# Performance work log

Hardware: AMD Instinct MI355X
Metric: run time of the kernel (lower is better)

Reference implementation:

```python
import jax, jax.numpy as jnp
import numpy as np

B, N, P, D = 16, 1024, 72, 96
ND, H, K = 64, 4, 16
LN_EPS = 1e-5
ROW_EPS = 1e-8


def topk_sparsify(adj, k):
    # adj: (..., N, N); keep top-k per row (scatter-mask), then row-renormalize
    shp = adj.shape
    n = shp[-1]
    flat = adj.reshape(-1, n)
    _, idx = jax.lax.top_k(flat, k)  # (R, k)
    rows = jnp.arange(flat.shape[0])[:, None]
    mask = jnp.zeros_like(flat).at[rows, idx].set(1.0)
    sp = flat * mask
    sp = sp / (sp.sum(-1, keepdims=True) + ROW_EPS)
    return sp.reshape(shp)


def setup_inputs() -> dict:
    key = jax.random.key(0)
    ks = jax.random.split(key, 12)
    xav1 = np.sqrt(6.0 / (N + ND))  # xavier_uniform bound for (N, ND)
    inp = {
        "patch_features": jax.random.normal(ks[0], (B, N, P, D), jnp.float32),
        "E1": jax.random.uniform(ks[1], (H, N, ND), jnp.float32, -xav1, xav1),
        "E2": jax.random.uniform(ks[2], (H, ND, N), jnp.float32, -xav1, xav1),
        "temperature": jnp.full((H,), 0.5, jnp.float32),
        "fusion_weight": jnp.float32(0.5),
        "dW1": jax.random.normal(ks[3], (D, ND), jnp.float32) / np.sqrt(D),
        "db1": jnp.zeros((ND,), jnp.float32),
        "ln_g": jnp.ones((ND,), jnp.float32),
        "ln_b": jnp.zeros((ND,), jnp.float32),
        "dW2": jax.random.normal(ks[4], (ND, ND), jnp.float32) / np.sqrt(ND),
        "db2": jnp.zeros((ND,), jnp.float32),
        "eW1": jax.random.normal(ks[5], (H, 2 * H), jnp.float32) / np.sqrt(H),
        "eb1": jnp.zeros((2 * H,), jnp.float32),
        "eW2": jax.random.normal(ks[6], (2 * H, 1), jnp.float32) / np.sqrt(2 * H),
        "eb2": jnp.zeros((1,), jnp.float32),
    }
    return inp


def reference(patch_features, E1, E2, temperature, fusion_weight,
              dW1, db1, ln_g, ln_b, dW2, db2, eW1, eb1, eW2, eb2):
    # ---- static multi-head graphs: softmax(relu(E1 @ E2) / T, axis=-1) ----
    s = jax.nn.relu(jnp.einsum('hnd,hdm->hnm', E1, E2))
    static_adjs = jax.nn.softmax(s / temperature[:, None, None], axis=-1)

    # ---- dynamic graphs from mean-pooled patch features ----
    node_repr = patch_features.mean(axis=2)                 # (B, N, D)
    h1 = node_repr @ dW1 + db1                              # (B, N, ND)
    mu = h1.mean(-1, keepdims=True)
    var = ((h1 - mu) ** 2).mean(-1, keepdims=True)
    h1 = (h1 - mu) / jnp.sqrt(var + LN_EPS) * ln_g + ln_b   # LayerNorm
    h1 = jax.nn.relu(h1)                                    # (dropout = identity, eval)
    dyn_emb = h1 @ dW2 + db2                                # (B, N, ND)
    d = jax.nn.relu(jnp.einsum('bnd,hdm->bhnm', dyn_emb, E2))
    dynamic_adjs = jax.nn.softmax(d / temperature[None, :, None, None], axis=-1)

    # ---- top-k sparsify + row renormalize ----
    static_adjs = topk_sparsify(static_adjs, K)             # (H, N, N)
    dynamic_adjs = topk_sparsify(dynamic_adjs, K)           # (B, H, N, N)

    # ---- fuse static + dynamic ----
    fused = (1.0 - fusion_weight) * static_adjs[None] + fusion_weight * dynamic_adjs

    # ---- edge MLP over head dim: (B, N, N, H) -> (B, N, N) ----
    x = jnp.transpose(fused, (0, 2, 3, 1))                  # (B, N, N, H)
    ew = jax.nn.relu(x @ eW1 + eb1) @ eW2 + eb2             # (B, N, N, 1)
    final_adjs = jax.nn.sigmoid(ew[..., 0]) * fused.mean(axis=1)
    return final_adjs, static_adjs, dynamic_adjs
```

## Files before the change

### kernel.cpp

```cpp
#include <hip/hip_runtime.h>

typedef unsigned int u32;
typedef unsigned long long u64;
typedef unsigned short u16;

#define Bn 16
#define Nn 1024
#define Pp 72
#define MARG 3e-4f

#define NEGINF __int_as_float(0xff800000)
#define POSINF __int_as_float(0x7f800000)

__device__ __forceinline__ float wsumf(float v) {
#pragma unroll
  for (int off = 1; off < 64; off <<= 1) v += __shfl_xor(v, off, 64);
  return v;
}
__device__ __forceinline__ float wmaxf(float v) {
#pragma unroll
  for (int off = 1; off < 64; off <<= 1) v = fmaxf(v, __shfl_xor(v, off, 64));
  return v;
}
__device__ __forceinline__ float wminf(float v) {
#pragma unroll
  for (int off = 1; off < 64; off <<= 1) v = fminf(v, __shfl_xor(v, off, 64));
  return v;
}
__device__ __forceinline__ u32 wminu(u32 v) {
#pragma unroll
  for (int off = 1; off < 64; off <<= 1) {
    u32 o = (u32)__shfl_xor((int)v, off, 64);
    v = (o < v) ? o : v;
  }
  return v;
}

__global__ __launch_bounds__(256) void k_e2t(const float* __restrict__ E2,
                                             float* __restrict__ E2T) {
  __shared__ float tile[32][65];
  const int h = blockIdx.x >> 5;
  const int m0 = (blockIdx.x & 31) << 5;
  const float* src = E2 + (size_t)h * 65536;
  float* dst = E2T + (size_t)h * 65536;
  const int t = threadIdx.x;
#pragma unroll
  for (int k = 0; k < 8; ++k) {
    int idx = k * 256 + t;
    int d = idx >> 5, mm = idx & 31;
    tile[mm][d] = src[d * 1024 + m0 + mm];
  }
  __syncthreads();
#pragma unroll
  for (int k = 0; k < 8; ++k) {
    int idx = k * 256 + t;
    int mm = idx >> 6, d = idx & 63;
    dst[(size_t)(m0 + mm) * 64 + d] = tile[mm][d];
  }
}

__global__ __launch_bounds__(128) void k_meanmlp(const float* __restrict__ pf,
                                                 const float* __restrict__ dW1,
                                                 const float* __restrict__ db1,
                                                 const float* __restrict__ ln_g,
                                                 const float* __restrict__ ln_b,
                                                 const float* __restrict__ dW2,
                                                 const float* __restrict__ db2,
                                                 double* __restrict__ embD,
                                                 float* __restrict__ embF) {
  __shared__ double ndD[96];
  __shared__ double red[64];
  __shared__ double h1r[64];
  const int t = threadIdx.x;
  const int bn = blockIdx.x;

  if (t < 96) {
    const float* src = pf + (size_t)bn * (Pp * 96) + t;
    double s = 0.0;
    for (int p = 0; p < Pp; ++p) s += (double)src[p * 96];
    ndD[t] = s / 72.0;
  }
  __syncthreads();

  double a = 0.0;
  if (t < 64) {
    a = (double)db1[t];
    for (int d = 0; d < 96; ++d) a = fma(ndD[d], (double)dW1[d * 64 + t], a);
    red[t] = a;
  }
  __syncthreads();
  for (int s2 = 32; s2 >= 1; s2 >>= 1) {
    if (t < s2) red[t] += red[t + s2];
    __syncthreads();
  }
  const double mu = red[0] * (1.0 / 64.0);
  __syncthreads();
  const double dv = a - mu;
  if (t < 64) red[t] = dv * dv;
  __syncthreads();
  for (int s2 = 32; s2 >= 1; s2 >>= 1) {
    if (t < s2) red[t] += red[t + s2];
    __syncthreads();
  }
  const double var = red[0] * (1.0 / 64.0);
  if (t < 64) {
    double xn = dv / sqrt(var + 1e-5) * (double)ln_g[t] + (double)ln_b[t];
    h1r[t] = xn > 0.0 ? xn : 0.0;
  }
  __syncthreads();
  if (t < 64) {
    double e = (double)db2[t];
    for (int k = 0; k < 64; ++k) e = fma(h1r[k], (double)dW2[k * 64 + t], e);
    embD[(size_t)bn * 64 + t] = e;
    embF[(size_t)bn * 64 + t] = (float)e;
  }
}

template <int MODE>
__global__ __launch_bounds__(256) void k_rows(const float* __restrict__ e1f,
                                              const double* __restrict__ embD,
                                              const float* __restrict__ embF,
                                              const float* __restrict__ E2,
                                              const float* __restrict__ E2T,
                                              const float* __restrict__ temp,
                                              float* __restrict__ outp) {
  __shared__ float lgA[8][1024];
  __shared__ float embsh[64][8];
  const int t = threadIdx.x;
  const int r0 = blockIdx.x * 8;
  int h;
  size_t erow;
  if (MODE == 0) {
    h = r0 >> 10;
    erow = (size_t)r0;
  } else {
    int b = r0 >> 12;
    h = (r0 >> 10) & 3;
    int n0 = r0 & 1023;
    erow = (size_t)(b << 10) + n0;
  }
  const float* efa = (MODE == 0) ? (e1f + erow * 64) : (embF + erow * 64);
  const float4* e2 = (const float4*)(E2 + (size_t)h * 65536);
  const float* e2t = E2T + (size_t)h * 65536;
  const float invT = 1.0f / temp[h];
  const double Td = (double)temp[h];

  for (int k = t; k < 512; k += 256) {
    int g = k & 7, d = k >> 3;
    embsh[d][g] = efa[g * 64 + d];
  }
  __syncthreads();

  float acc[8][4];
#pragma unroll
  for (int g = 0; g < 8; ++g)
#pragma unroll
    for (int x = 0; x < 4; ++x) acc[g][x] = 0.0f;

#pragma unroll 2
  for (int d = 0; d < 64; ++d) {
    float4 ev = e2[d * 256 + t];
    float4 sa = *(const float4*)&embsh[d][0];
    float4 sb = *(const float4*)&embsh[d][4];
    acc[0][0] = fmaf(sa.x, ev.x, acc[0][0]);
    acc[0][1] = fmaf(sa.x, ev.y, acc[0][1]);
    acc[0][2] = fmaf(sa.x, ev.z, acc[0][2]);
    acc[0][3] = fmaf(sa.x, ev.w, acc[0][3]);
    acc[1][0] = fmaf(sa.y, ev.x, acc[1][0]);
    acc[1][1] = fmaf(sa.y, ev.y, acc[1][1]);
    acc[1][2] = fmaf(sa.y, ev.z, acc[1][2]);
    acc[1][3] = fmaf(sa.y, ev.w, acc[1][3]);
    acc[2][0] = fmaf(sa.z, ev.x, acc[2][0]);
    acc[2][1] = fmaf(sa.z, ev.y, acc[2][1]);
    acc[2][2] = fmaf(sa.z, ev.z, acc[2][2]);
    acc[2][3] = fmaf(sa.z, ev.w, acc[2][3]);
    acc[3][0] = fmaf(sa.w, ev.x, acc[3][0]);
    acc[3][1] = fmaf(sa.w, ev.y, acc[3][1]);
    acc[3][2] = fmaf(sa.w, ev.z, acc[3][2]);
    acc[3][3] = fmaf(sa.w, ev.w, acc[3][3]);
    acc[4][0] = fmaf(sb.x, ev.x, acc[4][0]);
    acc[4][1] = fmaf(sb.x, ev.y, acc[4][1]);
    acc[4][2] = fmaf(sb.x, ev.z, acc[4][2]);
    acc[4][3] = fmaf(sb.x, ev.w, acc[4][3]);
    acc[5][0] = fmaf(sb.y, ev.x, acc[5][0]);
    acc[5][1] = fmaf(sb.y, ev.y, acc[5][1]);
    acc[5][2] = fmaf(sb.y, ev.z, acc[5][2]);
    acc[5][3] = fmaf(sb.y, ev.w, acc[5][3]);
    acc[6][0] = fmaf(sb.z, ev.x, acc[6][0]);
    acc[6][1] = fmaf(sb.z, ev.y, acc[6][1]);
    acc[6][2] = fmaf(sb.z, ev.z, acc[6][2]);
    acc[6][3] = fmaf(sb.z, ev.w, acc[6][3]);
    acc[7][0] = fmaf(sb.w, ev.x, acc[7][0]);
    acc[7][1] = fmaf(sb.w, ev.y, acc[7][1]);
    acc[7][2] = fmaf(sb.w, ev.z, acc[7][2]);
    acc[7][3] = fmaf(sb.w, ev.w, acc[7][3]);
  }
#pragma unroll
  for (int g = 0; g < 8; ++g) {
    float4 o;
    o.x = fmaxf(acc[g][0], 0.0f) * invT;
    o.y = fmaxf(acc[g][1], 0.0f) * invT;
    o.z = fmaxf(acc[g][2], 0.0f) * invT;
    o.w = fmaxf(acc[g][3], 0.0f) * invT;
    ((float4*)(&lgA[g][0]))[t] = o;
  }
  __syncthreads();

  const int w = t >> 6, l = t & 63;

#pragma unroll 1
  for (int gi = 0; gi < 2; ++gi) {
    const int g = w * 2 + gi;
    float q[16];
#pragma unroll
    for (int j = 0; j < 16; ++j) q[j] = lgA[g][l + (j << 6)];

    float lm = q[0];
#pragma unroll
    for (int j = 1; j < 16; ++j) lm = fmaxf(lm, q[j]);
    const float qmax = wmaxf(lm);

    u32 lo = 0u, hi = __float_as_uint(qmax) + 1u;
    u32 kept = 0u;
    bool f16 = false;
    float pvf = 0.0f;
#pragma unroll 1
    while (hi - lo > 1u) {
      u32 mid = (lo + hi) >> 1;
      float pv = __uint_as_float(mid);
      u32 cw = 0;
#pragma unroll
      for (int j = 0; j < 16; ++j)
        cw += (u32)__popcll(__ballot(q[j] >= pv));
      if (cw >= 16u) lo = mid; else hi = mid;
      if (cw == 16u) { f16 = true; pvf = pv; break; }
    }
    float theta, ub;
    if (f16) {
      float vmin = POSINF, umax = -1.0f;
#pragma unroll
      for (int j = 0; j < 16; ++j) {
        if (q[j] >= pvf) { kept |= 1u << j; vmin = fminf(vmin, q[j]); }
        else umax = fmaxf(umax, q[j]);
      }
      theta = wminf(vmin);
      ub = wmaxf(umax);
    } else {
      theta = __uint_as_float(lo);
      u32 cw = 0;
#pragma unroll
      for (int j = 0; j < 16; ++j) {
        u64 bj = __ballot(q[j] > theta);
        cw += (u32)__popcll(bj);
        if (q[j] > theta) kept |= 1u << j;
      }
      int r = 16 - (int)cw;
#pragma unroll 1
      for (int it = 0; it < r; ++it) {
        u32 mc = 0xFFFFFFFFu;
#pragma unroll
        for (int j = 0; j < 16; ++j)
          if (q[j] == theta && !((kept >> j) & 1u)) {
            u32 cc = (u32)((j << 6) | l);
            mc = cc < mc ? cc : mc;
          }
        u32 wm = wminu(mc);
        if ((wm & 63u) == (u32)l) kept |= 1u << (wm >> 6);
      }
      ub = theta;
    }

    if (theta - ub >= MARG) {
      float e[16];
      float es = 0.0f, ek = 0.0f;
#pragma unroll
      for (int j = 0; j < 16; ++j) {
        e[j] = __expf(q[j] - qmax);
        es += e[j];
        if ((kept >> j) & 1u) ek += e[j];
      }
      const float Z = wsumf(es);
      const float EK = wsumf(ek);
      const float inv = 1.0f / (EK + 1e-8f * Z);
#pragma unroll
      for (int j = 0; j < 16; ++j)
        lgA[g][l + (j << 6)] = ((kept >> j) & 1u) ? (e[j] * inv) : 0.0f;
    } else {
      double qd[16];
      const float thr = ub - MARG;
#pragma unroll 1
      for (int j = 0; j < 16; ++j) {
        if (q[j] >= thr) {
          const int m = l + (j << 6);
          const float* col = e2t + (size_t)m * 64;
          double a = 0.0;
          for (int d = 0; d < 64; ++d) {
            double s = (MODE == 0) ? (double)e1f[(erow + g) * 64 + d]
                                   : embD[(erow + g) * 64 + d];
            a = fma(s, (double)col[d], a);
          }
          qd[j] = (a > 0.0 ? a : 0.0) / Td;
        } else {
          qd[j] = (double)q[j];
        }
      }
      double bm = qd[0];
#pragma unroll
      for (int j = 1; j < 16; ++j) bm = qd[j] > bm ? qd[j] : bm;
      float mh = (float)bm;
      float mlo = (float)(bm - (double)mh);
      float whi = wmaxf(mh);
      float wlo = wmaxf(mh == whi ? mlo : NEGINF);
      const double qmaxd = (double)whi + (double)wlo;

      float ev2[16];
      float es2 = 0.0f;
#pragma unroll
      for (int j = 0; j < 16; ++j) { ev2[j] = __expf((float)(qd[j] - qmaxd)); es2 += ev2[j]; }
      const float Z2 = wsumf(es2);

      u32 kept2 = 0;
      float EK2 = 0.0f;
#pragma unroll 1
      for (int it = 0; it < 16; ++it) {
        double bv = -1.0;
        int bjj = -1;
#pragma unroll
        for (int j = 0; j < 16; ++j) {
          bool tk = (((kept2 >> j) & 1u) == 0u) && (qd[j] > bv);
          bv = tk ? qd[j] : bv;
          bjj = tk ? j : bjj;
        }
        float bh = NEGINF, bl = NEGINF;
        if (bjj >= 0) { bh = (float)bv; bl = (float)(bv - (double)bh); }
        float vhi = wmaxf(bh);
        float vlo = wmaxf(bh == vhi ? bl : NEGINF);
        bool elig = (bh == vhi) && (bl == vlo);
        u32 mc = elig ? (u32)((bjj << 6) | l) : 0xFFFFFFFFu;
        u32 mwin = wminu(mc);
        EK2 += __expf((float)(((double)vhi + (double)vlo) - qmaxd));
        if ((mwin & 63u) == (u32)l) kept2 |= 1u << (mwin >> 6);
      }
      const float inv2 = 1.0f / (EK2 + 1e-8f * Z2);
#pragma unroll
      for (int j = 0; j < 16; ++j)
        lgA[g][l + (j << 6)] = ((kept2 >> j) & 1u) ? (ev2[j] * inv2) : 0.0f;
    }
  }
  __syncthreads();

  float4* gout = (float4*)(outp + (size_t)r0 * 1024);
  const float4* src = (const float4*)(&lgA[0][0]);
#pragma unroll
  for (int k = 0; k < 8; ++k) {
    int i = t + k * 256;
    gout[i] = src[i];
  }
}

__global__ __launch_bounds__(256) void k_fuse(const float* __restrict__ dyn,
                                              const float* __restrict__ stat,
                                              float* __restrict__ fin,
                                              const float* __restrict__ eW1,
                                              const float* __restrict__ eb1,
                                              const float* __restrict__ eW2,
                                              const float* __restrict__ eb2,
                                              const float* __restrict__ fwp) {
  const float w = fwp[0];
  const float w1 = 1.0f - w;
  float W1[4][8], B1v[8], W2v[8];
#pragma unroll
  for (int hh = 0; hh < 4; ++hh)
#pragma unroll
    for (int j = 0; j < 8; ++j) W1[hh][j] = eW1[hh * 8 + j];
#pragma unroll
  for (int j = 0; j < 8; ++j) { B1v[j] = eb1[j]; W2v[j] = eW2[j]; }
  const float b2 = eb2[0];

  const int i = blockIdx.x * 256 + threadIdx.x;
  const int b = i >> 18;
  const int rem = i & 262143;
  const int n = rem >> 8;
  const int c4 = rem & 255;

  float fx[4][4];
#pragma unroll
  for (int hh = 0; hh < 4; ++hh) {
    float4 fd = ((const float4*)dyn)[(((size_t)((b * 4 + hh) * 1024 + n)) << 8) + c4];
    float4 fs = ((const float4*)stat)[(((size_t)(hh * 1024 + n)) << 8) + c4];
    fx[hh][0] = w1 * fs.x + w * fd.x;
    fx[hh][1] = w1 * fs.y + w * fd.y;
    fx[hh][2] = w1 * fs.z + w * fd.z;
    fx[hh][3] = w1 * fs.w + w * fd.w;
  }
  float ov[4];
#pragma unroll
  for (int x = 0; x < 4; ++x) {
    float ew = b2;
#pragma unroll
    for (int j = 0; j < 8; ++j) {
      float hj = B1v[j];
#pragma unroll
      for (int hh = 0; hh < 4; ++hh) hj = fmaf(fx[hh][x], W1[hh][j], hj);
      ew = fmaf(fmaxf(hj, 0.0f), W2v[j], ew);
    }
    float mean = (fx[0][x] + fx[1][x] + fx[2][x] + fx[3][x]) * 0.25f;
    float sg = 1.0f / (1.0f + __expf(-ew));
    ov[x] = sg * mean;
  }
  float4 o;
  o.x = ov[0]; o.y = ov[1]; o.z = ov[2]; o.w = ov[3];
  ((float4*)fin)[i] = o;
}

extern "C" void kernel_launch(void* const* d_in, const int* in_sizes, int n_in,
                              void* d_out, int out_size, void* d_ws, size_t ws_size,
                              hipStream_t stream) {
  const float* pf   = (const float*)d_in[0];
  const float* E1   = (const float*)d_in[1];
  const float* E2   = (const float*)d_in[2];
  const float* temp = (const float*)d_in[3];
  const float* fw   = (const float*)d_in[4];
  const float* dW1  = (const float*)d_in[5];
  const float* db1  = (const float*)d_in[6];
  const float* ln_g = (const float*)d_in[7];
  const float* ln_b = (const float*)d_in[8];
  const float* dW2  = (const float*)d_in[9];
  const float* db2  = (const float*)d_in[10];
  const float* eW1  = (const float*)d_in[11];
  const float* eb1  = (const float*)d_in[12];
  const float* eW2  = (const float*)d_in[13];
  const float* eb2  = (const float*)d_in[14];

  float* out_final = (float*)d_out;
  float* out_stat  = out_final + (size_t)Bn * Nn * Nn;
  float* out_dyn   = out_stat + (size_t)4 * Nn * Nn;

  double* embD = (double*)d_out;
  float* embF = out_final + 2097152;
  float* E2T  = out_final + 3145728;

  k_e2t<<<128, 256, 0, stream>>>(E2, E2T);
  k_meanmlp<<<Bn * Nn, 128, 0, stream>>>(pf, dW1, db1, ln_g, ln_b, dW2, db2, embD, embF);
  k_rows<0><<<512, 256, 0, stream>>>(E1, nullptr, nullptr, E2, E2T, temp, out_stat);
  k_rows<1><<<8192, 256, 0, stream>>>(nullptr, embD, embF, E2, E2T, temp, out_dyn);
  k_fuse<<<16384, 256, 0, stream>>>(out_dyn, out_stat, out_final, eW1, eb1, eW2, eb2, fw);
}
```

Before: 662.8 us.

## Use 512-thread row blocks with one row per wave and DPP reductions

```diff
diff --git a/kernel.cpp b/kernel.cpp
--- a/kernel.cpp
+++ b/kernel.cpp
@@ -12,21 +12,28 @@
 #define NEGINF __int_as_float(0xff800000)
 #define POSINF __int_as_float(0x7f800000)
 
-__device__ __forceinline__ float wsumf(float v) {
-#pragma unroll
-  for (int off = 1; off < 64; off <<= 1) v += __shfl_xor(v, off, 64);
-  return v;
-}
-__device__ __forceinline__ float wmaxf(float v) {
-#pragma unroll
-  for (int off = 1; off < 64; off <<= 1) v = fmaxf(v, __shfl_xor(v, off, 64));
-  return v;
-}
-__device__ __forceinline__ float wminf(float v) {
-#pragma unroll
-  for (int off = 1; off < 64; off <<= 1) v = fminf(v, __shfl_xor(v, off, 64));
-  return v;
-}
+#define DPP_STEP(OP, CTRL, RM)                                                 \
+  y = __builtin_amdgcn_update_dpp(__float_as_int(v), __float_as_int(v),        \
+                                  CTRL, RM, 0xf, false);                       \
+  v = OP(v, __int_as_float(y));
+
+#define DPP_RED(NAME, OP)                                                      \
+  __device__ __forceinline__ float NAME(float v) {                             \
+    int y;                                                                     \
+    DPP_STEP(OP, 0x111, 0xf)                                                   \
+    DPP_STEP(OP, 0x112, 0xf)                                                   \
+    DPP_STEP(OP, 0x114, 0xf)                                                   \
+    DPP_STEP(OP, 0x118, 0xf)                                                   \
+    DPP_STEP(OP, 0x142, 0xa)                                                   \
+    DPP_STEP(OP, 0x143, 0xc)                                                   \
+    return __int_as_float(__builtin_amdgcn_readlane(__float_as_int(v), 63));   \
+  }
+
+#define FADDOP(a, b) ((a) + (b))
+DPP_RED(dmaxf, fmaxf)
+DPP_RED(dminf, fminf)
+DPP_RED(dsumf, FADDOP)
+
 __device__ __forceinline__ u32 wminu(u32 v) {
 #pragma unroll
   for (int off = 1; off < 64; off <<= 1) {
@@ -117,7 +124,7 @@
 }
 
 template <int MODE>
-__global__ __launch_bounds__(256) void k_rows(const float* __restrict__ e1f,
+__global__ __launch_bounds__(512) void k_rows(const float* __restrict__ e1f,
                                               const double* __restrict__ embD,
                                               const float* __restrict__ embF,
                                               const float* __restrict__ E2,
@@ -140,77 +147,55 @@
     erow = (size_t)(b << 10) + n0;
   }
   const float* efa = (MODE == 0) ? (e1f + erow * 64) : (embF + erow * 64);
-  const float4* e2 = (const float4*)(E2 + (size_t)h * 65536);
+  const float2* e2 = (const float2*)(E2 + (size_t)h * 65536);
   const float* e2t = E2T + (size_t)h * 65536;
   const float invT = 1.0f / temp[h];
   const double Td = (double)temp[h];
 
-  for (int k = t; k < 512; k += 256) {
-    int g = k & 7, d = k >> 3;
+  {
+    int g = t & 7, d = t >> 3;
     embsh[d][g] = efa[g * 64 + d];
   }
   __syncthreads();
 
-  float acc[8][4];
-#pragma unroll
-  for (int g = 0; g < 8; ++g)
-#pragma unroll
-    for (int x = 0; x < 4; ++x) acc[g][x] = 0.0f;
-
-#pragma unroll 2
+  float acc[8][2];
+#pragma unroll
+  for (int g = 0; g < 8; ++g) { acc[g][0] = 0.0f; acc[g][1] = 0.0f; }
+
+#pragma unroll 4
   for (int d = 0; d < 64; ++d) {
-    float4 ev = e2[d * 256 + t];
+    float2 ev = e2[d * 512 + t];
     float4 sa = *(const float4*)&embsh[d][0];
     float4 sb = *(const float4*)&embsh[d][4];
     acc[0][0] = fmaf(sa.x, ev.x, acc[0][0]);
     acc[0][1] = fmaf(sa.x, ev.y, acc[0][1]);
-    acc[0][2] = fmaf(sa.x, ev.z, acc[0][2]);
-    acc[0][3] = fmaf(sa.x, ev.w, acc[0][3]);
     acc[1][0] = fmaf(sa.y, ev.x, acc[1][0]);
     acc[1][1] = fmaf(sa.y, ev.y, acc[1][1]);
-    acc[1][2] = fmaf(sa.y, ev.z, acc[1][2]);
-    acc[1][3] = fmaf(sa.y, ev.w, acc[1][3]);
     acc[2][0] = fmaf(sa.z, ev.x, acc[2][0]);
     acc[2][1] = fmaf(sa.z, ev.y, acc[2][1]);
-    acc[2][2] = fmaf(sa.z, ev.z, acc[2][2]);
-    acc[2][3] = fmaf(sa.z, ev.w, acc[2][3]);
     acc[3][0] = fmaf(sa.w, ev.x, acc[3][0]);
     acc[3][1] = fmaf(sa.w, ev.y, acc[3][1]);
-    acc[3][2] = fmaf(sa.w, ev.z, acc[3][2]);
-    acc[3][3] = fmaf(sa.w, ev.w, acc[3][3]);
     acc[4][0] = fmaf(sb.x, ev.x, acc[4][0]);
     acc[4][1] = fmaf(sb.x, ev.y, acc[4][1]);
-    acc[4][2] = fmaf(sb.x, ev.z, acc[4][2]);
-    acc[4][3] = fmaf(sb.x, ev.w, acc[4][3]);
     acc[5][0] = fmaf(sb.y, ev.x, acc[5][0]);
     acc[5][1] = fmaf(sb.y, ev.y, acc[5][1]);
-    acc[5][2] = fmaf(sb.y, ev.z, acc[5][2]);
-    acc[5][3] = fmaf(sb.y, ev.w, acc[5][3]);
     acc[6][0] = fmaf(sb.z, ev.x, acc[6][0]);
     acc[6][1] = fmaf(sb.z, ev.y, acc[6][1]);
-    acc[6][2] = fmaf(sb.z, ev.z, acc[6][2]);
-    acc[6][3] = fmaf(sb.z, ev.w, acc[6][3]);
     acc[7][0] = fmaf(sb.w, ev.x, acc[7][0]);
     acc[7][1] = fmaf(sb.w, ev.y, acc[7][1]);
-    acc[7][2] = fmaf(sb.w, ev.z, acc[7][2]);
-    acc[7][3] = fmaf(sb.w, ev.w, acc[7][3]);
   }
 #pragma unroll
   for (int g = 0; g < 8; ++g) {
-    float4 o;
+    float2 o;
     o.x = fmaxf(acc[g][0], 0.0f) * invT;
     o.y = fmaxf(acc[g][1], 0.0f) * invT;
-    o.z = fmaxf(acc[g][2], 0.0f) * invT;
-    o.w = fmaxf(acc[g][3], 0.0f) * invT;
-    ((float4*)(&lgA[g][0]))[t] = o;
+    ((float2*)(&lgA[g][0]))[t] = o;
   }
   __syncthreads();
 
   const int w = t >> 6, l = t & 63;
-
-#pragma unroll 1
-  for (int gi = 0; gi < 2; ++gi) {
-    const int g = w * 2 + gi;
+  {
+    const int g = w;
     float q[16];
 #pragma unroll
     for (int j = 0; j < 16; ++j) q[j] = lgA[g][l + (j << 6)];
@@ -218,7 +203,7 @@
     float lm = q[0];
 #pragma unroll
     for (int j = 1; j < 16; ++j) lm = fmaxf(lm, q[j]);
-    const float qmax = wmaxf(lm);
+    const float qmax = dmaxf(lm);
 
     u32 lo = 0u, hi = __float_as_uint(qmax) + 1u;
     u32 kept = 0u;
@@ -243,15 +228,14 @@
         if (q[j] >= pvf) { kept |= 1u << j; vmin = fminf(vmin, q[j]); }
         else umax = fmaxf(umax, q[j]);
       }
-      theta = wminf(vmin);
-      ub = wmaxf(umax);
+      theta = dminf(vmin);
+      ub = dmaxf(umax);
     } else {
       theta = __uint_as_float(lo);
       u32 cw = 0;
 #pragma unroll
       for (int j = 0; j < 16; ++j) {
-        u64 bj = __ballot(q[j] > theta);
-        cw += (u32)__popcll(bj);
+        cw += (u32)__popcll(__ballot(q[j] > theta));
         if (q[j] > theta) kept |= 1u << j;
       }
       int r = 16 - (int)cw;
@@ -279,8 +263,8 @@
         es += e[j];
         if ((kept >> j) & 1u) ek += e[j];
       }
-      const float Z = wsumf(es);
-      const float EK = wsumf(ek);
+      const float Z = dsumf(es);
+      const float EK = dsumf(ek);
       const float inv = 1.0f / (EK + 1e-8f * Z);
 #pragma unroll
       for (int j = 0; j < 16; ++j)
@@ -309,15 +293,15 @@
       for (int j = 1; j < 16; ++j) bm = qd[j] > bm ? qd[j] : bm;
       float mh = (float)bm;
       float mlo = (float)(bm - (double)mh);
-      float whi = wmaxf(mh);
-      float wlo = wmaxf(mh == whi ? mlo : NEGINF);
+      float whi = dmaxf(mh);
+      float wlo = dmaxf(mh == whi ? mlo : NEGINF);
       const double qmaxd = (double)whi + (double)wlo;
 
       float ev2[16];
       float es2 = 0.0f;
 #pragma unroll
       for (int j = 0; j < 16; ++j) { ev2[j] = __expf((float)(qd[j] - qmaxd)); es2 += ev2[j]; }
-      const float Z2 = wsumf(es2);
+      const float Z2 = dsumf(es2);
 
       u32 kept2 = 0;
       float EK2 = 0.0f;
@@ -333,8 +317,8 @@
         }
         float bh = NEGINF, bl = NEGINF;
         if (bjj >= 0) { bh = (float)bv; bl = (float)(bv - (double)bh); }
-        float vhi = wmaxf(bh);
-        float vlo = wmaxf(bh == vhi ? bl : NEGINF);
+        float vhi = dmaxf(bh);
+        float vlo = dmaxf(bh == vhi ? bl : NEGINF);
         bool elig = (bh == vhi) && (bl == vlo);
         u32 mc = elig ? (u32)((bjj << 6) | l) : 0xFFFFFFFFu;
         u32 mwin = wminu(mc);
@@ -352,8 +336,8 @@
   float4* gout = (float4*)(outp + (size_t)r0 * 1024);
   const float4* src = (const float4*)(&lgA[0][0]);
 #pragma unroll
-  for (int k = 0; k < 8; ++k) {
-    int i = t + k * 256;
+  for (int k = 0; k < 4; ++k) {
+    int i = t + k * 512;
     gout[i] = src[i];
   }
 }
@@ -442,7 +426,7 @@
 
   k_e2t<<<128, 256, 0, stream>>>(E2, E2T);
   k_meanmlp<<<Bn * Nn, 128, 0, stream>>>(pf, dW1, db1, ln_g, ln_b, dW2, db2, embD, embF);
-  k_rows<0><<<512, 256, 0, stream>>>(E1, nullptr, nullptr, E2, E2T, temp, out_stat);
-  k_rows<1><<<8192, 256, 0, stream>>>(nullptr, embD, embF, E2, E2T, temp, out_dyn);
+  k_rows<0><<<512, 512, 0, stream>>>(E1, nullptr, nullptr, E2, E2T, temp, out_stat);
+  k_rows<1><<<8192, 512, 0, stream>>>(nullptr, embD, embF, E2, E2T, temp, out_dyn);
   k_fuse<<<16384, 256, 0, stream>>>(out_dyn, out_stat, out_final, eW1, eb1, eW2, eb2, fw);
 }
```

Measured after the change: 604.5 us. 1.1x faster.
